# Kernel optimization log

Measured on AMD Instinct MI355X. Metric: run time of the kernel, lower is better.

The kernel has to match this reference:

```python
import jax, jax.numpy as jnp
import numpy as np

B, T, F = 512, 256, 64
H = [128, 256, 128, 64]

def _glorot(key, shape):
    fan_in, fan_out = shape[0], shape[1]
    lim = np.sqrt(6.0 / (fan_in + fan_out))
    return jax.random.uniform(key, shape, jnp.float32, -lim, lim)

def setup_inputs() -> dict:
    key = jax.random.key(0)
    ks = jax.random.split(key, 16)
    inp = {"x": jax.random.normal(ks[0], (B, T, F), jnp.float32)}
    dims = [F] + H
    for i in range(4):
        inp[f"Wx{i+1}"] = _glorot(ks[1 + 3 * i], (dims[i], dims[i + 1]))
        # keras uses orthogonal recurrent init; scaled normal is an acceptable stand-in
        q, _ = jnp.linalg.qr(jax.random.normal(ks[2 + 3 * i], (dims[i + 1], dims[i + 1])))
        inp[f"Wh{i+1}"] = q.astype(jnp.float32)
        inp[f"b{i+1}"] = jnp.zeros((dims[i + 1],), jnp.float32)
    inp["Wd"] = _glorot(ks[13], (T * H[-1], 1))
    inp["bd"] = jnp.zeros((1,), jnp.float32)
    return inp

def simple_rnn(x, Wx, Wh, b):
    # x: [B, T, Fin] -> hidden sequence [B, T, H]; h_t = relu(x_t Wx + h_{t-1} Wh + b)
    xp = jnp.einsum('btf,fh->tbh', x, Wx) + b  # precompute input projection, time-major
    h0 = jnp.zeros((x.shape[0], Wh.shape[0]), x.dtype)
    def step(h, xt):
        h = jax.nn.relu(xt + h @ Wh)
        return h, h
    _, hs = jax.lax.scan(step, h0, xp)  # hs: [T, B, H]
    return jnp.transpose(hs, (1, 0, 2))

def reference(x, Wx1, Wh1, b1, Wx2, Wh2, b2, Wx3, Wh3, b3, Wx4, Wh4, b4, Wd, bd):
    h = simple_rnn(x, Wx1, Wh1, b1)   # dropout layers are identity at inference
    h = simple_rnn(h, Wx2, Wh2, b2)
    h = simple_rnn(h, Wx3, Wh3, b3)
    h = simple_rnn(h, Wx4, Wh4, b4)
    flat = h.reshape(h.shape[0], -1)  # [B, T*64]
    return flat @ Wd + bd             # [B, 1]
```

## Files before the change

kernel.cpp:

```cpp
#include <hip/hip_runtime.h>
#include <hip/hip_bf16.h>

#define BB 512
#define TT 256

typedef __attribute__((ext_vector_type(8))) short bf16x8;
typedef __attribute__((ext_vector_type(4))) float f32x4;

__device__ __forceinline__ unsigned short f2b(float f) {
    union { float f; unsigned u; } v; v.f = f;
    unsigned r = v.u + 0x7FFFu + ((v.u >> 16) & 1u);
    return (unsigned short)(r >> 16);
}
__device__ __forceinline__ float b2f(unsigned short h) {
    union { unsigned u; float f; } v; v.u = ((unsigned)h) << 16;
    return v.f;
}
__device__ __forceinline__ ushort2 pk2(float a, float b) {
    __hip_bfloat162 h = __float22bfloat162_rn(float2{a, b});
    union { __hip_bfloat162 h; ushort2 u; } v; v.h = h; return v.u;
}


__global__ __launch_bounds__(256) void cvt_tile4(const float* __restrict__ x,
                                                 unsigned short* __restrict__ xb) {
    __shared__ float xs[16][260];
    const int s = blockIdx.x >> 6;
    const int tg = blockIdx.x & 63;
    const int tid = threadIdx.x;
    const float* xbase = x + ((size_t)(s * 16) * TT + tg * 4) * 64;
#pragma unroll
    for (int it = 0; it < 4; ++it) {
        const int b = it * 4 + (tid >> 6);
        const int r = tid & 63;
        float4 v = *reinterpret_cast<const float4*>(xbase + (size_t)b * (TT * 64) + r * 4);
        *reinterpret_cast<float4*>(&xs[b][r * 4]) = v;
    }
    __syncthreads();
#pragma unroll
    for (int it = 0; it < 2; ++it) {
        const int t = it * 2 + (tid >> 7);
        const int oct = (tid >> 4) & 7;
        const int b = tid & 15;
        const float* src = &xs[b][t * 64 + oct * 8];
        float4 va = *reinterpret_cast<const float4*>(src);
        float4 vb = *reinterpret_cast<const float4*>(src + 4);
        ushort2 p0 = pk2(va.x, va.y), p1 = pk2(va.z, va.w);
        ushort2 p2 = pk2(vb.x, vb.y), p3 = pk2(vb.z, vb.w);
        ushort4 lo; lo.x = p0.x; lo.y = p0.y; lo.z = p1.x; lo.w = p1.y;
        ushort4 hi; hi.x = p2.x; hi.y = p2.y; hi.z = p3.x; hi.w = p3.y;
        unsigned short* ob = xb + ((size_t)(s * TT) + tg * 4 + t) * 1024 + oct * 128 + b * 8;
        *reinterpret_cast<ushort4*>(ob) = lo;
        *reinterpret_cast<ushort4*>(ob + 4) = hi;
    }
}

__global__ __launch_bounds__(512) __attribute__((amdgpu_waves_per_eu(2, 2))) void rnn4(
    const unsigned short* __restrict__ Xb,
    const float* __restrict__ Wx1, const float* __restrict__ Wh1, const float* __restrict__ b1,
    const float* __restrict__ Wx2, const float* __restrict__ Wh2, const float* __restrict__ b2,
    const float* __restrict__ Wx3, const float* __restrict__ Wh3, const float* __restrict__ b3,
    const float* __restrict__ Wx4, const float* __restrict__ Wh4, const float* __restrict__ b4,
    unsigned short* __restrict__ H4,
    const float* __restrict__ Wd, const float* __restrict__ bd,
    float* __restrict__ out) {
    const int tid = threadIdx.x;
    const int s = blockIdx.x;
    const int w = tid >> 6;
    const int lane = tid & 63;
    const int l15 = lane & 15;
    const int quad = lane >> 4;
    const int rdo = quad * 128 + l15 * 8;

    __shared__ __align__(16) unsigned short hall[2][9216];

    bf16x8 wreg[48];
    f32x4 bvv[6];

#define LOADW(BASE, WP, H_, CB, KC_, MT_)                                          \
    _Pragma("unroll")                                                              \
    for (int mt = 0; mt < MT_; ++mt) {                                             \
        int m = (CB) + mt * 16 + l15;                                              \
        _Pragma("unroll")                                                          \
        for (int kc = 0; kc < KC_; ++kc)                                           \
            _Pragma("unroll")                                                      \
            for (int j = 0; j < 8; ++j)                                            \
                wreg[(BASE) + kc * MT_ + mt][j] =                                  \
                    (short)f2b(WP[(kc * 32 + quad * 8 + j) * H_ + m]);             \
    }
#define LOADBF(OFF, BP, CB, MT_)                                                   \
    _Pragma("unroll")                                                              \
    for (int mt = 0; mt < MT_; ++mt) {                                             \
        float4 t4v = *reinterpret_cast<const float4*>((BP) + (CB) + mt * 16 + quad * 4); \
        bvv[(OFF) + mt][0] = t4v.x; bvv[(OFF) + mt][1] = t4v.y;                    \
        bvv[(OFF) + mt][2] = t4v.z; bvv[(OFF) + mt][3] = t4v.w;                    \
    }

    if (w < 2) {
        LOADW(0,  Wh1, 128, w * 64, 4, 4)
        LOADW(16, Wx1, 128, w * 64, 2, 4)
        LOADW(24, Wh4, 64,  w * 32, 2, 2)
        LOADW(28, Wx4, 64,  w * 32, 4, 2)
        LOADBF(0, b1, w * 64, 4)
        LOADBF(4, b4, w * 32, 2)
    } else if (w < 6) {
        __builtin_amdgcn_s_setprio(1);
        LOADW(0,  Wh2, 256, (w - 2) * 64, 8, 4)
        LOADW(32, Wx2, 256, (w - 2) * 64, 4, 4)
        LOADBF(0, b2, (w - 2) * 64, 4)
    } else {
        LOADW(0,  Wh3, 128, (w - 6) * 64, 4, 4)
        LOADW(16, Wx3, 128, (w - 6) * 64, 8, 4)
        LOADBF(0, b3, (w - 6) * 64, 4)
    }
#undef LOADW
#undef LOADBF

    for (int i = tid; i < 2 * 9216; i += 512) (&hall[0][0])[i] = 0;

    const unsigned short* Xs = Xb + (size_t)s * TT * 1024;
    unsigned short* H4s = H4 + (size_t)s * TT * 1024;

    if (w < 2) {
#pragma unroll
        for (int kx = 0; kx < 2; ++kx) {
            wreg[36 + kx] = *reinterpret_cast<const bf16x8*>(&Xs[kx * 512 + rdo]);
            wreg[38 + kx] = *reinterpret_cast<const bf16x8*>(&Xs[1024 + kx * 512 + rdo]);
        }
    }
    __syncthreads();

    const unsigned short* xp0 = Xs + 2 * 1024 + rdo;
    const unsigned short* xp1 = Xs + 3 * 1024 + rdo;

    const int wro1 = (w * 8 + (quad >> 1)) * 128 + l15 * 8 + (quad & 1) * 4;
    const int wro4 = 8192 + (w * 4 + (quad >> 1)) * 128 + l15 * 8 + (quad & 1) * 4;
    const int wro2 = 2048 + ((w - 2) * 8 + (quad >> 1)) * 128 + l15 * 8 + (quad & 1) * 4;
    const int wro3 = 6144 + ((w - 6) * 8 + (quad >> 1)) * 128 + l15 * 8 + (quad & 1) * 4;

    unsigned short* op_e = H4s + 1024 + (wro4 - 8192);
    unsigned short* op_o = H4s + (wro4 - 8192);

#define PACKMK(ACC_MT)                                                             \
    ushort2 lo = pk2(fmaxf((ACC_MT)[0], 0.f), fmaxf((ACC_MT)[1], 0.f));            \
    ushort2 hi = pk2(fmaxf((ACC_MT)[2], 0.f), fmaxf((ACC_MT)[3], 0.f));            \
    ushort4 o; o.x = lo.x; o.y = lo.y; o.z = hi.x; o.w = hi.y;

#define STEP(TAU_, RP_, WP_, XAB, XPP, OPP)                                        \
    {                                                                              \
        const int tau_ = (TAU_);                                                   \
        const unsigned short* RB = &hall[RP_][0];                                  \
        unsigned short* WB = &hall[WP_][0];                                        \
        if (w < 2) {                                                               \
            if ((unsigned)tau_ < TT) {                                     \
                f32x4 acc[4];                                                      \
                _Pragma("unroll")                                                  \
                for (int mt = 0; mt < 4; ++mt)                                     \
                    acc[mt] = __builtin_amdgcn_mfma_f32_16x16x32_bf16(             \
                        wreg[16 + mt], wreg[(XAB) + 0], bvv[mt], 0, 0, 0);         \
                _Pragma("unroll")                                                  \
                for (int mt = 0; mt < 4; ++mt)                                     \
                    acc[mt] = __builtin_amdgcn_mfma_f32_16x16x32_bf16(             \
                        wreg[20 + mt], wreg[(XAB) + 1], acc[mt], 0, 0, 0);         \
                if (tau_ + 2 < TT) {                                               \
                    wreg[(XAB) + 0] = *reinterpret_cast<const bf16x8*>(XPP);       \
                    wreg[(XAB) + 1] = *reinterpret_cast<const bf16x8*>(XPP + 512); \
                    XPP += 2048;                                                   \
                }                                                                  \
                _Pragma("unroll")                                                  \
                for (int kc = 0; kc < 4; ++kc) {                                   \
                    bf16x8 af = *reinterpret_cast<const bf16x8*>(&RB[rdo + kc * 512]); \
                    _Pragma("unroll")                                              \
                    for (int mt = 0; mt < 4; ++mt)                                 \
                        acc[mt] = __builtin_amdgcn_mfma_f32_16x16x32_bf16(         \
                            wreg[kc * 4 + mt], af, acc[mt], 0, 0, 0);              \
                }                                                                  \
                _Pragma("unroll")                                                  \
                for (int mt = 0; mt < 4; ++mt) {                                   \
                    PACKMK(acc[mt])                                                \
                    *reinterpret_cast<ushort4*>(&WB[wro1 + mt * 256]) = o;         \
                }                                                                  \
            }                                                                      \
            if ((unsigned)(tau_ - 3) < TT) {                               \
                f32x4 acc[2];                                                      \
                {                                                                  \
                    bf16x8 af0 = *reinterpret_cast<const bf16x8*>(&RB[6144 + rdo]); \
                    _Pragma("unroll")                                              \
                    for (int mt = 0; mt < 2; ++mt)                                 \
                        acc[mt] = __builtin_amdgcn_mfma_f32_16x16x32_bf16(         \
                            wreg[28 + mt], af0, bvv[4 + mt], 0, 0, 0);             \
                }                                                                  \
                _Pragma("unroll")                                                  \
                for (int kx = 1; kx < 4; ++kx) {                                   \
                    bf16x8 af = *reinterpret_cast<const bf16x8*>(&RB[6144 + rdo + kx * 512]); \
                    _Pragma("unroll")                                              \
                    for (int mt = 0; mt < 2; ++mt)                                 \
                        acc[mt] = __builtin_amdgcn_mfma_f32_16x16x32_bf16(         \
                            wreg[28 + kx * 2 + mt], af, acc[mt], 0, 0, 0);         \
                }                                                                  \
                _Pragma("unroll")                                                  \
                for (int kc = 0; kc < 2; ++kc) {                                   \
                    bf16x8 af = *reinterpret_cast<const bf16x8*>(&RB[8192 + rdo + kc * 512]); \
                    _Pragma("unroll")                                              \
                    for (int mt = 0; mt < 2; ++mt)                                 \
                        acc[mt] = __builtin_amdgcn_mfma_f32_16x16x32_bf16(         \
                            wreg[24 + kc * 2 + mt], af, acc[mt], 0, 0, 0);         \
                }                                                                  \
                _Pragma("unroll")                                                  \
                for (int mt = 0; mt < 2; ++mt) {                                   \
                    PACKMK(acc[mt])                                                \
                    *reinterpret_cast<ushort4*>(&WB[wro4 + mt * 256]) = o;         \
                    *reinterpret_cast<ushort4*>(OPP + mt * 256) = o;               \
                }                                                                  \
                OPP += 2048;                                                       \
            }                                                                      \
        } else if (w < 6) {                                                        \
            if ((unsigned)(tau_ - 1) < TT) {                               \
                f32x4 acc[4];                                                      \
                {                                                                  \
                    bf16x8 af0 = *reinterpret_cast<const bf16x8*>(&RB[rdo]);       \
                    _Pragma("unroll")                                              \
                    for (int mt = 0; mt < 4; ++mt)                                 \
                        acc[mt] = __builtin_amdgcn_mfma_f32_16x16x32_bf16(         \
                            wreg[32 + mt], af0, bvv[mt], 0, 0, 0);                 \
                }                                                                  \
                _Pragma("unroll")                                                  \
                for (int kx = 1; kx < 4; ++kx) {                                   \
                    bf16x8 af = *reinterpret_cast<const bf16x8*>(&RB[rdo + kx * 512]); \
                    _Pragma("unroll")                                              \
                    for (int mt = 0; mt < 4; ++mt)                                 \
                        acc[mt] = __builtin_amdgcn_mfma_f32_16x16x32_bf16(         \
                            wreg[32 + kx * 4 + mt], af, acc[mt], 0, 0, 0);         \
                }                                                                  \
                _Pragma("unroll")                                                  \
                for (int kc = 0; kc < 8; ++kc) {                                   \
                    bf16x8 af = *reinterpret_cast<const bf16x8*>(&RB[2048 + rdo + kc * 512]); \
                    _Pragma("unroll")                                              \
                    for (int mt = 0; mt < 4; ++mt)                                 \
                        acc[mt] = __builtin_amdgcn_mfma_f32_16x16x32_bf16(         \
                            wreg[kc * 4 + mt], af, acc[mt], 0, 0, 0);              \
                }                                                                  \
                _Pragma("unroll")                                                  \
                for (int mt = 0; mt < 4; ++mt) {                                   \
                    PACKMK(acc[mt])                                                \
                    *reinterpret_cast<ushort4*>(&WB[wro2 + mt * 256]) = o;         \
                }                                                                  \
            }                                                                      \
        } else {                                                                   \
            if ((unsigned)(tau_ - 2) < TT) {                               \
                f32x4 acc[4];                                                      \
                {                                                                  \
                    bf16x8 af0 = *reinterpret_cast<const bf16x8*>(&RB[2048 + rdo]); \
                    _Pragma("unroll")                                              \
                    for (int mt = 0; mt < 4; ++mt)                                 \
                        acc[mt] = __builtin_amdgcn_mfma_f32_16x16x32_bf16(         \
                            wreg[16 + mt], af0, bvv[mt], 0, 0, 0);                 \
                }                                                                  \
                _Pragma("unroll")                                                  \
                for (int kx = 1; kx < 8; ++kx) {                                   \
                    bf16x8 af = *reinterpret_cast<const bf16x8*>(&RB[2048 + rdo + kx * 512]); \
                    _Pragma("unroll")                                              \
                    for (int mt = 0; mt < 4; ++mt)                                 \
                        acc[mt] = __builtin_amdgcn_mfma_f32_16x16x32_bf16(         \
                            wreg[16 + kx * 4 + mt], af, acc[mt], 0, 0, 0);         \
                }                                                                  \
                _Pragma("unroll")                                                  \
                for (int kc = 0; kc < 4; ++kc) {                                   \
                    bf16x8 af = *reinterpret_cast<const bf16x8*>(&RB[6144 + rdo + kc * 512]); \
                    _Pragma("unroll")                                              \
                    for (int mt = 0; mt < 4; ++mt)                                 \
                        acc[mt] = __builtin_amdgcn_mfma_f32_16x16x32_bf16(         \
                            wreg[kc * 4 + mt], af, acc[mt], 0, 0, 0);              \
                }                                                                  \
                _Pragma("unroll")                                                  \
                for (int mt = 0; mt < 4; ++mt) {                                   \
                    PACKMK(acc[mt])                                                \
                    *reinterpret_cast<ushort4*>(&WB[wro3 + mt * 256]) = o;         \
                }                                                                  \
            }                                                                      \
        }                                                                          \
        __builtin_amdgcn_s_waitcnt(0xC07F);                                        \
        __builtin_amdgcn_s_barrier();                                              \
    }

#pragma unroll 1
    for (int tau = 0; tau < TT + 3; tau += 2) {
        STEP(tau, 0, 1, 36, xp0, op_e)
        STEP(tau + 1, 1, 0, 38, xp1, op_o)
    }
#undef STEP
#undef PACKMK

    __builtin_amdgcn_s_waitcnt(0x0F70);
    __syncthreads();
    {
        float dacc = 0.f;
        const unsigned short* gb = H4s + quad * 128 + l15 * 8;
        const float* wb = Wd + quad * 8;
#pragma unroll 4
        for (int ti = 0; ti < 32; ++ti) {
            const int t = w + ti * 8;
            bf16x8 h0 = *reinterpret_cast<const bf16x8*>(gb + (size_t)t * 1024);
            bf16x8 h1 = *reinterpret_cast<const bf16x8*>(gb + (size_t)t * 1024 + 512);
            const float* wd = wb + t * 64;
            float4 wa = *reinterpret_cast<const float4*>(wd);
            float4 wc = *reinterpret_cast<const float4*>(wd + 4);
            float4 we = *reinterpret_cast<const float4*>(wd + 32);
            float4 wg = *reinterpret_cast<const float4*>(wd + 36);
            dacc += b2f((unsigned short)h0[0]) * wa.x + b2f((unsigned short)h0[1]) * wa.y +
                    b2f((unsigned short)h0[2]) * wa.z + b2f((unsigned short)h0[3]) * wa.w +
                    b2f((unsigned short)h0[4]) * wc.x + b2f((unsigned short)h0[5]) * wc.y +
                    b2f((unsigned short)h0[6]) * wc.z + b2f((unsigned short)h0[7]) * wc.w +
                    b2f((unsigned short)h1[0]) * we.x + b2f((unsigned short)h1[1]) * we.y +
                    b2f((unsigned short)h1[2]) * we.z + b2f((unsigned short)h1[3]) * we.w +
                    b2f((unsigned short)h1[4]) * wg.x + b2f((unsigned short)h1[5]) * wg.y +
                    b2f((unsigned short)h1[6]) * wg.z + b2f((unsigned short)h1[7]) * wg.w;
        }
        float* red = reinterpret_cast<float*>(&hall[0][0]);
        red[(w * 4 + quad) * 16 + l15] = dacc;
        __syncthreads();
        if (tid < 16) {
            float sum = bd[0];
#pragma unroll
            for (int j = 0; j < 32; ++j) sum += red[j * 16 + tid];
            out[s * 16 + tid] = sum;
        }
    }
}

extern "C" void kernel_launch(void* const* d_in, const int* in_sizes, int n_in,
                              void* d_out, int out_size, void* d_ws, size_t ws_size,
                              hipStream_t stream) {
    (void)in_sizes; (void)n_in; (void)out_size; (void)ws_size;
    const float* x   = (const float*)d_in[0];
    const float* Wx1 = (const float*)d_in[1];
    const float* Wh1 = (const float*)d_in[2];
    const float* b1  = (const float*)d_in[3];
    const float* Wx2 = (const float*)d_in[4];
    const float* Wh2 = (const float*)d_in[5];
    const float* b2  = (const float*)d_in[6];
    const float* Wx3 = (const float*)d_in[7];
    const float* Wh3 = (const float*)d_in[8];
    const float* b3  = (const float*)d_in[9];
    const float* Wx4 = (const float*)d_in[10];
    const float* Wh4 = (const float*)d_in[11];
    const float* b4  = (const float*)d_in[12];
    const float* Wd  = (const float*)d_in[13];
    const float* bd  = (const float*)d_in[14];
    float* out = (float*)d_out;

    char* ws = (char*)d_ws;
    unsigned short* xbT = (unsigned short*)(ws);
    unsigned short* H4  = (unsigned short*)(ws + 16777216);

    cvt_tile4<<<2048, 256, 0, stream>>>(x, xbT);

    rnn4<<<32, 512, 0, stream>>>(xbT, Wx1, Wh1, b1, Wx2, Wh2, b2,
                                 Wx3, Wh3, b3, Wx4, Wh4, b4, H4, Wd, bd, out);
}
```

Before: 423.5 us.

## Replace per-step block barrier with LDS progress flags and triple-buffered hidden state

Each wave group now waits only on the producer and consumer waves it depends on, polling per-wave progress counters in shared memory, instead of a full workgroup barrier every timestep. The hidden-state buffer goes from double to triple buffering so waves can run up to a step apart without overwriting data that is still being read. This is meant to cut barrier stalls between unevenly loaded layer waves. In exchange it adds spin-polling overhead and memory-ordering risk, since LDS visibility relies on waitcnt plus volatile flag stores.

```diff
diff --git a/kernel.cpp b/kernel.cpp
--- a/kernel.cpp
+++ b/kernel.cpp
@@ -72,7 +72,8 @@
     const int quad = lane >> 4;
     const int rdo = quad * 128 + l15 * 8;
 
-    __shared__ __align__(16) unsigned short hall[2][9216];
+    __shared__ __align__(16) unsigned short hall[3][9216];
+    __shared__ int prog[8];
 
     bf16x8 wreg[48];
     f32x4 bvv[6];
@@ -116,7 +117,8 @@
 #undef LOADW
 #undef LOADBF
 
-    for (int i = tid; i < 2 * 9216; i += 512) (&hall[0][0])[i] = 0;
+    for (int i = tid; i < 3 * 9216; i += 512) (&hall[0][0])[i] = 0;
+    if (tid < 8) prog[tid] = -1;
 
     const unsigned short* Xs = Xb + (size_t)s * TT * 1024;
     unsigned short* H4s = H4 + (size_t)s * TT * 1024;
@@ -146,12 +148,36 @@
     ushort2 hi = pk2(fmaxf((ACC_MT)[2], 0.f), fmaxf((ACC_MT)[3], 0.f));            \
     ushort4 o; o.x = lo.x; o.y = lo.y; o.z = hi.x; o.w = hi.y;
 
-#define STEP(TAU_, RP_, WP_, XAB, XPP, OPP)                                        \
+#define POLL(I_, M1_, M2_)                                                         \
+    {                                                                              \
+        int thr_;                                                                  \
+        if (lane < 8)                                                              \
+            thr_ = (((M1_) >> lane) & 1) ? (I_) - 1                                \
+                 : ((((M2_) >> lane) & 1) ? (I_) - 2 : (int)0x80000000);           \
+        else                                                                       \
+            thr_ = (int)0x80000000;                                                \
+        while (true) {                                                             \
+            int v_ = *(volatile int*)&prog[lane & 7];                              \
+            if (__all(v_ >= thr_)) break;                                          \
+            __builtin_amdgcn_s_sleep(1);                                           \
+        }                                                                          \
+        asm volatile("" ::: "memory");                                             \
+    }
+
+#define PUBLISH(I_)                                                                \
+    asm volatile("" ::: "memory");                                                 \
+    __builtin_amdgcn_s_waitcnt(0xC07F);                                            \
+    asm volatile("" ::: "memory");                                                 \
+    if (lane == 0) *(volatile int*)&prog[w] = (I_);                                \
+    asm volatile("" ::: "memory");
+
+#define STEP(TAU_, RBP_, WBP_, XAB, XPP, OPP)                                      \
     {                                                                              \
         const int tau_ = (TAU_);                                                   \
-        const unsigned short* RB = &hall[RP_][0];                                  \
-        unsigned short* WB = &hall[WP_][0];                                        \
+        const unsigned short* RB = (RBP_);                                         \
+        unsigned short* WB = (WBP_);                                               \
         if (w < 2) {                                                               \
+            POLL(tau_, 0xC3, 0x3F)                                                 \
             if ((unsigned)tau_ < TT) {                                     \
                 f32x4 acc[4];                                                      \
                 _Pragma("unroll")                                                  \
@@ -215,6 +241,7 @@
                 OPP += 2048;                                                       \
             }                                                                      \
         } else if (w < 6) {                                                        \
+            POLL(tau_, 0x3F, 0xFC)                                                 \
             if ((unsigned)(tau_ - 1) < TT) {                               \
                 f32x4 acc[4];                                                      \
                 {                                                                  \
@@ -247,6 +274,7 @@
                 }                                                                  \
             }                                                                      \
         } else {                                                                   \
+            POLL(tau_, 0xFC, 0xC3)                                                 \
             if ((unsigned)(tau_ - 2) < TT) {                               \
                 f32x4 acc[4];                                                      \
                 {                                                                  \
@@ -279,16 +307,23 @@
                 }                                                                  \
             }                                                                      \
         }                                                                          \
-        __builtin_amdgcn_s_waitcnt(0xC07F);                                        \
-        __builtin_amdgcn_s_barrier();                                              \
-    }
+        PUBLISH(tau_)                                                              \
+    }
+
+    unsigned short* bprv = &hall[2][0];
+    unsigned short* bcur = &hall[0][0];
+    unsigned short* bnxt = &hall[1][0];
 
 #pragma unroll 1
     for (int tau = 0; tau < TT + 3; tau += 2) {
-        STEP(tau, 0, 1, 36, xp0, op_e)
-        STEP(tau + 1, 1, 0, 38, xp1, op_o)
+        STEP(tau, bprv, bcur, 36, xp0, op_e)
+        { unsigned short* t_ = bprv; bprv = bcur; bcur = bnxt; bnxt = t_; }
+        STEP(tau + 1, bprv, bcur, 38, xp1, op_o)
+        { unsigned short* t_ = bprv; bprv = bcur; bcur = bnxt; bnxt = t_; }
     }
 #undef STEP
+#undef POLL
+#undef PUBLISH
 #undef PACKMK
 
     __builtin_amdgcn_s_waitcnt(0x0F70);
```

Result: slower. 475.7 us (+12.3%).
